# Performance work log

Hardware: AMD Instinct MI355X
Metric: run time of the kernel (lower is better)

The kernel has to match this reference:

```python
import jax, jax.numpy as jnp
import numpy as np

HEAD_NUM = 8
HEAD_DIM = 32
EPS = 0.0  # torch.linalg.norm division has no eps; keep exact


def setup_inputs() -> dict:
    key = jax.random.key(0)
    k1, k2 = jax.random.split(key)
    batch_s = jax.random.normal(k1, (2048, HEAD_NUM * HEAD_DIM), dtype=jnp.float32)
    batch_ro = jax.random.normal(k2, (8192, HEAD_NUM * HEAD_DIM), dtype=jnp.float32)
    return {"batch_s": batch_s, "batch_ro": batch_ro}


def reference(batch_s, batch_ro):
    N, M = batch_s.shape[0], batch_ro.shape[0]
    s = batch_s.reshape(N, HEAD_NUM, HEAD_DIM)   # [N, H, D]
    ro = batch_ro.reshape(M, HEAD_NUM, HEAD_DIM)  # [M, H, D]
    # L2-normalize each head vector
    s = s / jnp.linalg.norm(s, axis=-1, keepdims=True)
    ro = ro / jnp.linalg.norm(ro, axis=-1, keepdims=True)
    # per-head cosine similarity: [N, M, H]
    dist = jnp.einsum('nhd,mhd->nmh', s, ro)
    # max-pool over heads -> [N, M]
    return jnp.max(dist, axis=-1)
```

## Files before the change

### kernel.cpp

```cpp
#include <hip/hip_runtime.h>

#define S_ROWS 2048
#define RO_ROWS 8192
#define HEADS 8
#define HDIM 32
#define ROWLEN 256
#define NB_S (S_ROWS / 16)
#define NB_RO (RO_ROWS / 16)

typedef __attribute__((ext_vector_type(8))) short bf16x8;
typedef __attribute__((ext_vector_type(4))) float f32x4;
typedef __attribute__((ext_vector_type(4))) short s16x4;

__device__ __forceinline__ short f32_to_bf16_rne(float f) {
    union { float f; unsigned u; } v; v.f = f;
    return (short)((v.u + 0x7fffu + ((v.u >> 16) & 1u)) >> 16);
}

__global__ __launch_bounds__(256) void mhd_normalize(const float* __restrict__ s,
                                                     const float* __restrict__ ro,
                                                     short* __restrict__ sF,
                                                     short* __restrict__ roF) {
    const int v   = blockIdx.x * 256 + threadIdx.x;
    const int dg  = v & 7;
    const int r16 = (v >> 3) & 15;
    const int u   = v >> 7;
    const int h   = u & 7;
    const int nb_all = u >> 3;
    const bool isS = nb_all < NB_S;
    const int nb  = isS ? nb_all : nb_all - NB_S;
    const int n   = nb * 16 + r16;

    const float* src = isS ? s : ro;
    f32x4 x = *(const f32x4*)(src + (size_t)n * ROWLEN + h * HDIM + dg * 4);
    float ss = x[0] * x[0] + x[1] * x[1] + x[2] * x[2] + x[3] * x[3];
    ss += __shfl_xor(ss, 1);
    ss += __shfl_xor(ss, 2);
    ss += __shfl_xor(ss, 4);
    const float inv = rsqrtf(ss);
    s16x4 r;
    r[0] = f32_to_bf16_rne(x[0] * inv);
    r[1] = f32_to_bf16_rne(x[1] * inv);
    r[2] = f32_to_bf16_rne(x[2] * inv);
    r[3] = f32_to_bf16_rne(x[3] * inv);

    short* dst = isS ? sF : roF;
    const int NB = isS ? NB_S : NB_RO;
    const int lane_in_frag = ((dg >> 1) << 4) + r16;
    const size_t off = ((size_t)(h * NB + nb) << 9) + lane_in_frag * 8 + (dg & 1) * 4;
    *(s16x4*)(dst + off) = r;
}

__global__ __launch_bounds__(512, 4) void mhd_dist(const short* __restrict__ sF,
                                                   const short* __restrict__ roF,
                                                   float* __restrict__ out) {
    __shared__ float elds[8][16][68];
    const int lane = threadIdx.x & 63;
    const int wave = threadIdx.x >> 6;
    const int wr = wave >> 1;
    const int wc = wave & 1;
    const int xcd = blockIdx.x & 7;
    const int q   = blockIdx.x >> 3;
    const int nbA = xcd * 16 + wr * 4;
    const int nbB = q * 8 + wc * 4;
    const size_t laneOff = (size_t)lane * 8;

    const int l15 = lane & 15;
    const int kg = lane >> 4;
    float* outBase = out + (size_t)(xcd * 256 + wr * 64) * RO_ROWS
                         + q * 128 + wc * 64;
    const int srow = lane >> 4;
    const int scol = (lane & 15) * 4;

#pragma unroll 1
    for (int i = 0; i < 4; ++i) {
        f32x4 rmax[4];
#pragma unroll
        for (int j = 0; j < 4; ++j)
            rmax[j] = (f32x4){-3.0e38f, -3.0e38f, -3.0e38f, -3.0e38f};

#pragma unroll 1
        for (int h = 0; h < HEADS; ++h) {
            const bf16x8 a = *(const bf16x8*)(
                sF + ((size_t)(h * NB_S + nbA + i) << 9) + laneOff);
            const short* bBase = roF + ((size_t)(h * NB_RO + nbB) << 9) + laneOff;
            bf16x8 b[4];
#pragma unroll
            for (int j = 0; j < 4; ++j)
                b[j] = *(const bf16x8*)(bBase + ((size_t)j << 9));
#pragma unroll
            for (int j = 0; j < 4; ++j) {
                f32x4 acc = {0.f, 0.f, 0.f, 0.f};
                acc = __builtin_amdgcn_mfma_f32_16x16x32_bf16(b[j], a, acc, 0, 0, 0);
#pragma unroll
                for (int q2 = 0; q2 < 4; ++q2)
                    rmax[j][q2] = fmaxf(rmax[j][q2], acc[q2]);
            }
        }

#pragma unroll
        for (int j = 0; j < 4; ++j)
            *(f32x4*)&elds[wave][l15][kg * 4 + j * 16] = rmax[j];
#pragma unroll
        for (int t = 0; t < 4; ++t) {
            const int rowL = t * 4 + srow;
            f32x4 vv = *(const f32x4*)&elds[wave][rowL][scol];
            *(f32x4*)(outBase + (size_t)(i * 16 + rowL) * RO_ROWS + scol) = vv;
        }
    }
}

extern "C" void kernel_launch(void* const* d_in, const int* in_sizes, int n_in,
                              void* d_out, int out_size, void* d_ws, size_t ws_size,
                              hipStream_t stream) {
    const float* batch_s  = (const float*)d_in[0];
    const float* batch_ro = (const float*)d_in[1];
    float* out = (float*)d_out;

    short* sF  = (short*)d_ws;
    short* roF = sF + (size_t)S_ROWS * ROWLEN;

    const int totalV4 = (S_ROWS + RO_ROWS) * ROWLEN / 4;
    mhd_normalize<<<totalV4 / 256, 256, 0, stream>>>(batch_s, batch_ro, sF, roF);

    mhd_dist<<<(S_ROWS / 256) * (RO_ROWS / 128), 512, 0, stream>>>(sF, roF, out);
}
```

Measured before the change: 106.7 us.

## Stage ro tile in LDS via global_load_lds and retile blocks to 512x64

Restructures the distance kernel so each block covers 512 s rows by 64 ro columns. The block's ro fragments for all heads are loaded once into LDS with direct global-to-LDS loads and then reused by all waves. Each wave now processes two s fragments per ro fragment to get more register reuse. The LDS transpose staging for the output is dropped in favour of direct strided f32x4 stores, and launch bounds are raised to 8 for occupancy. The risk is less coalesced output writes, and the larger ro-tile LDS footprint may limit occupancy.

```diff
diff --git a/kernel.cpp b/kernel.cpp
--- a/kernel.cpp
+++ b/kernel.cpp
@@ -15,6 +15,12 @@
 __device__ __forceinline__ short f32_to_bf16_rne(float f) {
     union { float f; unsigned u; } v; v.f = f;
     return (short)((v.u + 0x7fffu + ((v.u >> 16) & 1u)) >> 16);
+}
+
+__device__ __forceinline__ void gll16(const void* g, void* l) {
+    __builtin_amdgcn_global_load_lds(
+        (const __attribute__((address_space(1))) unsigned*)g,
+        (__attribute__((address_space(3))) unsigned*)l, 16, 0, 0);
 }
 
 __global__ __launch_bounds__(256) void mhd_normalize(const float* __restrict__ s,
@@ -51,62 +57,63 @@
     *(s16x4*)(dst + off) = r;
 }
 
-__global__ __launch_bounds__(512, 4) void mhd_dist(const short* __restrict__ sF,
+__global__ __launch_bounds__(512, 8) void mhd_dist(const short* __restrict__ sF,
                                                    const short* __restrict__ roF,
                                                    float* __restrict__ out) {
-    __shared__ float elds[8][16][68];
+    __shared__ short ldsB[32 * 512];
     const int lane = threadIdx.x & 63;
     const int wave = threadIdx.x >> 6;
-    const int wr = wave >> 1;
-    const int wc = wave & 1;
-    const int xcd = blockIdx.x & 7;
-    const int q   = blockIdx.x >> 3;
-    const int nbA = xcd * 16 + wr * 4;
-    const int nbB = q * 8 + wc * 4;
+    const int rowTile = blockIdx.x & 3;
+    const int colTile = blockIdx.x >> 2;
     const size_t laneOff = (size_t)lane * 8;
 
+#pragma unroll
+    for (int r = 0; r < 4; ++r)
+        gll16(roF + (((size_t)(wave * NB_RO + colTile * 4 + r)) << 9) + laneOff,
+              &ldsB[(size_t)(wave * 4 + r) << 9]);
+    __syncthreads();
+
+    const int nbA = rowTile * 32 + wave * 4;
     const int l15 = lane & 15;
     const int kg = lane >> 4;
-    float* outBase = out + (size_t)(xcd * 256 + wr * 64) * RO_ROWS
-                         + q * 128 + wc * 64;
-    const int srow = lane >> 4;
-    const int scol = (lane & 15) * 4;
+    float* outW = out + (size_t)(rowTile * 512 + wave * 64) * RO_ROWS
+                      + colTile * 64;
 
 #pragma unroll 1
-    for (int i = 0; i < 4; ++i) {
-        f32x4 rmax[4];
+    for (int p = 0; p < 2; ++p) {
+        f32x4 rmax[2][4];
 #pragma unroll
-        for (int j = 0; j < 4; ++j)
-            rmax[j] = (f32x4){-3.0e38f, -3.0e38f, -3.0e38f, -3.0e38f};
+        for (int c = 0; c < 2; ++c)
+#pragma unroll
+            for (int j = 0; j < 4; ++j)
+                rmax[c][j] = (f32x4){-3.0e38f, -3.0e38f, -3.0e38f, -3.0e38f};
 
 #pragma unroll 1
         for (int h = 0; h < HEADS; ++h) {
-            const bf16x8 a = *(const bf16x8*)(
-                sF + ((size_t)(h * NB_S + nbA + i) << 9) + laneOff);
-            const short* bBase = roF + ((size_t)(h * NB_RO + nbB) << 9) + laneOff;
-            bf16x8 b[4];
-#pragma unroll
-            for (int j = 0; j < 4; ++j)
-                b[j] = *(const bf16x8*)(bBase + ((size_t)j << 9));
+            const short* aCol = sF + (((size_t)(h * NB_S + nbA + p * 2)) << 9) + laneOff;
+            const bf16x8 a0 = *(const bf16x8*)(aCol);
+            const bf16x8 a1 = *(const bf16x8*)(aCol + 512);
 #pragma unroll
             for (int j = 0; j < 4; ++j) {
-                f32x4 acc = {0.f, 0.f, 0.f, 0.f};
-                acc = __builtin_amdgcn_mfma_f32_16x16x32_bf16(b[j], a, acc, 0, 0, 0);
+                const bf16x8 b = *(const bf16x8*)&ldsB[(((size_t)(h * 4 + j)) << 9) + laneOff];
+                f32x4 t0 = {0.f, 0.f, 0.f, 0.f};
+                f32x4 t1 = {0.f, 0.f, 0.f, 0.f};
+                t0 = __builtin_amdgcn_mfma_f32_16x16x32_bf16(b, a0, t0, 0, 0, 0);
+                t1 = __builtin_amdgcn_mfma_f32_16x16x32_bf16(b, a1, t1, 0, 0, 0);
 #pragma unroll
-                for (int q2 = 0; q2 < 4; ++q2)
-                    rmax[j][q2] = fmaxf(rmax[j][q2], acc[q2]);
+                for (int q = 0; q < 4; ++q) {
+                    rmax[0][j][q] = fmaxf(rmax[0][j][q], t0[q]);
+                    rmax[1][j][q] = fmaxf(rmax[1][j][q], t1[q]);
+                }
             }
         }
 
 #pragma unroll
-        for (int j = 0; j < 4; ++j)
-            *(f32x4*)&elds[wave][l15][kg * 4 + j * 16] = rmax[j];
+        for (int c = 0; c < 2; ++c)
 #pragma unroll
-        for (int t = 0; t < 4; ++t) {
-            const int rowL = t * 4 + srow;
-            f32x4 vv = *(const f32x4*)&elds[wave][rowL][scol];
-            *(f32x4*)(outBase + (size_t)(i * 16 + rowL) * RO_ROWS + scol) = vv;
-        }
+            for (int j = 0; j < 4; ++j)
+                *(f32x4*)(outW + (size_t)(p * 32 + c * 16 + l15) * RO_ROWS
+                          + j * 16 + kg * 4) = rmax[c][j];
     }
 }
 
@@ -123,5 +130,5 @@
     const int totalV4 = (S_ROWS + RO_ROWS) * ROWLEN / 4;
     mhd_normalize<<<totalV4 / 256, 256, 0, stream>>>(batch_s, batch_ro, sF, roF);
 
-    mhd_dist<<<(S_ROWS / 256) * (RO_ROWS / 128), 512, 0, stream>>>(sF, roF, out);
+    mhd_dist<<<(S_ROWS / 512) * (RO_ROWS / 64), 512, 0, stream>>>(sF, roF, out);
 }
```

Result: faster. 100.6 us (-5.7%).
